# Performance work log

Hardware: AMD Instinct MI355X
Metric: run time of the kernel (lower is better)

## Reference

```python
import jax, jax.numpy as jnp
import numpy as np

N = 50000
E = 800000
DESC = 256
IN_CH = DESC + 64  # 320
HEADS = 4
HC = 64  # hidden_channels // heads
HID = HEADS * HC  # 256


def _lin(k, fan_in, fan_out):
    kw, kb = jax.random.split(k)
    s = 1.0 / np.sqrt(fan_in)
    W = jax.random.uniform(kw, (fan_in, fan_out), minval=-s, maxval=s, dtype=jnp.float32)
    b = jax.random.uniform(kb, (fan_out,), minval=-s, maxval=s, dtype=jnp.float32)
    return W, b


def setup_inputs() -> dict:
    key = jax.random.key(0)
    ks = jax.random.split(key, 16)
    x = jax.random.normal(ks[0], (N, DESC), dtype=jnp.float32)
    kpts = jax.random.uniform(ks[1], (N, 2), dtype=jnp.float32) * jnp.array([1216.0, 352.0])
    pts_3d = jax.random.uniform(ks[2], (N, 3), dtype=jnp.float32) * 10.0
    edge_index = jax.random.randint(ks[3], (2, E), 0, N, dtype=jnp.int64)

    W1, b1 = _lin(ks[4], 3, 32)
    W2, b2 = _lin(ks[5], 32, 64)
    Wres, bres = _lin(ks[6], IN_CH, HID)
    Wl, bl = _lin(ks[7], IN_CH, HID)
    Wr, br = _lin(ks[8], IN_CH, HID)
    We, _ = _lin(ks[9], 3, HID)
    att = jax.random.normal(ks[10], (HEADS, HC), dtype=jnp.float32) * 0.1
    conv_bias = jnp.zeros((HID,), dtype=jnp.float32)
    gamma = jnp.ones((HID,), dtype=jnp.float32)
    beta = jnp.zeros((HID,), dtype=jnp.float32)
    Wp, bp = _lin(ks[11], HID, 256)
    return dict(x=x, kpts=kpts, pts_3d=pts_3d, edge_index=edge_index,
                W1=W1, b1=b1, W2=W2, b2=b2, Wres=Wres, bres=bres,
                Wl=Wl, bl=bl, Wr=Wr, br=br, We=We, att=att, conv_bias=conv_bias,
                gamma=gamma, beta=beta, Wp=Wp, bp=bp)


def reference(x, kpts, pts_3d, edge_index, W1, b1, W2, b2, Wres, bres,
              Wl, bl, Wr, br, We, att, conv_bias, gamma, beta, Wp, bp):
    n = x.shape[0]
    norm_uv = kpts / jnp.array([1216.0, 352.0], dtype=kpts.dtype)
    depth = pts_3d[:, 2:3]
    pos_input = jnp.concatenate([norm_uv, depth], axis=-1)  # [N,3]
    pos_feat = jax.nn.silu(pos_input @ W1 + b1) @ W2 + b2   # [N,64]
    node_x = jnp.concatenate([x, pos_feat], axis=-1)        # [N,320]

    src, dst = edge_index[0], edge_index[1]
    rel_uv = norm_uv[dst] - norm_uv[src]                    # [E,2]
    dist = jnp.linalg.norm(rel_uv, axis=-1, keepdims=True)  # [E,1]
    edge_attr = jnp.concatenate([rel_uv, dist], axis=-1)    # [E,3]

    identity = node_x @ Wres + bres                         # [N,256]

    # GATv2Conv (share_weights=False, concat=True, neg_slope=0.2, no self-loops)
    x_l = (node_x @ Wl + bl).reshape(n, HEADS, HC)
    x_r = (node_x @ Wr + br).reshape(n, HEADS, HC)
    e_feat = (edge_attr @ We).reshape(-1, HEADS, HC)        # [E,H,C]

    m = x_l[src] + x_r[dst] + e_feat                        # [E,H,C]
    m = jnp.where(m >= 0, m, 0.2 * m)                       # LeakyReLU(0.2)
    logits = jnp.einsum('ehc,hc->eh', m, att)               # [E,H]

    # segment softmax over incoming edges of each dst node
    lmax = jax.ops.segment_max(logits, dst, num_segments=n)  # [N,H]
    ex = jnp.exp(logits - lmax[dst])
    denom = jax.ops.segment_sum(ex, dst, num_segments=n)     # [N,H]
    alpha = ex / (denom[dst] + 1e-16)                        # [E,H]

    msg = x_l[src] * alpha[:, :, None]                       # [E,H,C]
    out = jax.ops.segment_sum(msg, dst, num_segments=n).reshape(n, HID) + conv_bias

    # LayerNorm
    mu = out.mean(-1, keepdims=True)
    var = out.var(-1, keepdims=True)
    out = (out - mu) / jnp.sqrt(var + 1e-5) * gamma + beta

    out = jax.nn.silu(out)
    out = out + identity
    out = out @ Wp + bp
    return out, alpha
```

## Files before the change

kernel.cpp:

```cpp
#include <hip/hip_runtime.h>
#include <math.h>

#define NN 50000
#define NPAD 50048
#define EE 800000
#define HIDC 256
#define INCH 320

typedef __attribute__((ext_vector_type(8))) short bf16x8;
typedef __attribute__((ext_vector_type(4))) float f32x4;
typedef __attribute__((ext_vector_type(2))) float f32x2;

static __device__ __forceinline__ float4 ld4(const float* p){ return *(const float4*)p; }

static __device__ __forceinline__ unsigned short f2b(float f){
  union { float f; unsigned u; } v; v.f = f;
  unsigned r = v.u + 0x7fffu + ((v.u >> 16) & 1u);
  return (unsigned short)(r >> 16);
}
static __device__ __forceinline__ float b2f(unsigned short u){
  union { unsigned u; float f; } v; v.u = ((unsigned)u) << 16; return v.f;
}
static __device__ __forceinline__ f32x2 unpk(unsigned u){
  f32x2 r;
  r.x = __uint_as_float(u << 16);
  r.y = __uint_as_float(u & 0xffff0000u);
  return r;
}
static __device__ __forceinline__ f32x2 fma2(f32x2 a, f32x2 b, f32x2 c){
  return __builtin_elementwise_fma(a, b, c);
}
static __device__ __forceinline__ f32x2 max2(f32x2 a, f32x2 b){
  return __builtin_elementwise_max(a, b);
}
static __device__ __forceinline__ f32x2 set2(float v){ f32x2 r; r.x = v; r.y = v; return r; }

typedef const __attribute__((address_space(1))) unsigned int* gas_u32;
typedef __attribute__((address_space(3))) unsigned int* las_u32;
static __device__ __forceinline__ void gload_lds16(const void* g, void* l){
  __builtin_amdgcn_global_load_lds((gas_u32)g, (las_u32)l, 16, 0, 0);
}

__global__ void cvt_x_kernel(const float* __restrict__ x, unsigned short* __restrict__ nodex)
{
  int t = blockIdx.x*blockDim.x + threadIdx.x;
  int row = t >> 6;
  if (row >= NN) return;
  int c4 = (t & 63) * 4;
  float4 v = ld4(x + (size_t)row*256 + c4);
  ushort4 o;
  o.x = f2b(v.x); o.y = f2b(v.y); o.z = f2b(v.z); o.w = f2b(v.w);
  *(ushort4*)(nodex + (size_t)row*320 + c4) = o;
}

__global__ void node_mlp_kernel(const float* __restrict__ kpts,
                                const float* __restrict__ pts3d,
                                const float* __restrict__ W1, const float* __restrict__ b1,
                                const float* __restrict__ W2, const float* __restrict__ b2,
                                unsigned short* __restrict__ nodex)
{
  int i = blockIdx.x*blockDim.x + threadIdx.x;
  if (i >= NN) return;
  float u = kpts[2*i]   * (1.0f/1216.0f);
  float v = kpts[2*i+1] * (1.0f/352.0f);
  float d = pts3d[3*i+2];
  float h[32];
#pragma unroll
  for (int j=0;j<32;++j){
    float t = u*W1[j] + v*W1[32+j] + d*W1[64+j] + b1[j];
    h[j] = t / (1.0f + __expf(-t));
  }
  for (int o=0;o<64;o+=4){
    float s0=b2[o], s1=b2[o+1], s2=b2[o+2], s3=b2[o+3];
#pragma unroll
    for (int j=0;j<32;++j){
      float hj = h[j];
      const float* w = W2 + j*64 + o;
      s0 += hj*w[0]; s1 += hj*w[1]; s2 += hj*w[2]; s3 += hj*w[3];
    }
    ushort4 r; r.x=f2b(s0); r.y=f2b(s1); r.z=f2b(s2); r.w=f2b(s3);
    *(ushort4*)(nodex + (size_t)i*320 + 256 + o) = r;
  }
}

__global__ void cvt_w_kernel(const float* __restrict__ Wres, const float* __restrict__ Wl,
                             const float* __restrict__ Wr,   const float* __restrict__ Wp,
                             const float* __restrict__ bres, const float* __restrict__ bl,
                             const float* __restrict__ br,
                             unsigned short* __restrict__ wt, float* __restrict__ biascat)
{
  int t = blockIdx.x*blockDim.x + threadIdx.x;
  if (t < 245760) {
    int which = t / 81920;
    int rem = t % 81920;
    int n = rem / 320, k = rem % 320;
    const float* W = (which == 0) ? Wres : (which == 1) ? Wl : Wr;
    wt[(size_t)which*81920 + rem] = f2b(W[(size_t)k*256 + n]);
  } else if (t < 311296) {
    int r = t - 245760;
    int n = r / 256, k = r % 256;
    wt[245760 + r] = f2b(Wp[(size_t)k*256 + n]);
  } else {
    int r = t - 311296;
    const float* src = (r < 256) ? bres : (r < 512) ? bl : br;
    biascat[r] = src[r & 255];
  }
}

#define GK 32
__global__ __launch_bounds__(256) void mfma_gemm_kernel(
    const unsigned short* __restrict__ A,
    const unsigned short* __restrict__ BT,
    const float* __restrict__ bias,
    float* __restrict__ Cf,
    unsigned short* __restrict__ Cx1,
    unsigned short* __restrict__ Cx2,
    int M, int K)
{
  __shared__ unsigned short Als[128*GK];
  __shared__ unsigned short Bls[128*GK];
  int tid = threadIdx.x;
  int lane = tid & 63, wave = tid >> 6;
  int wm = (wave >> 1) * 64, wn = (wave & 1) * 64;
  int row0 = blockIdx.x * 128, col0 = blockIdx.y * 128;

  f32x4 acc[4][4];
#pragma unroll
  for (int i=0;i<4;++i)
#pragma unroll
    for (int j=0;j<4;++j){ acc[i][j].x=0.f; acc[i][j].y=0.f; acc[i][j].z=0.f; acc[i][j].w=0.f; }

  int fm = lane & 15;
  int fk = (lane >> 4) * 8;

  for (int k0 = 0; k0 < K; k0 += GK) {
#pragma unroll
    for (int it = 0; it < 2; ++it) {
      int seg = it*256 + tid;
      int r = seg >> 2, kb = (seg & 3) * 8;
      gload_lds16(A  + (size_t)(row0 + r)*K + k0 + kb, Als + (it*256 + wave*64)*8);
      gload_lds16(BT + (size_t)(col0 + r)*K + k0 + kb, Bls + (it*256 + wave*64)*8);
    }
    __syncthreads();

    bf16x8 af[4], bfr[4];
#pragma unroll
    for (int mi=0; mi<4; ++mi)
      af[mi] = *(const bf16x8*)&Als[(wm + mi*16 + fm)*GK + fk];
#pragma unroll
    for (int ni=0; ni<4; ++ni)
      bfr[ni] = *(const bf16x8*)&Bls[(wn + ni*16 + fm)*GK + fk];
#pragma unroll
    for (int mi=0; mi<4; ++mi)
#pragma unroll
      for (int ni=0; ni<4; ++ni)
        acc[mi][ni] = __builtin_amdgcn_mfma_f32_16x16x32_bf16(af[mi], bfr[ni], acc[mi][ni], 0, 0, 0);
    __syncthreads();
  }

  int seg = col0 >> 8;
  int colbase = col0 - seg*256;
  int cn = lane & 15, cr = (lane >> 4) * 4;
#pragma unroll
  for (int ni=0; ni<4; ++ni){
    int gcol = col0 + wn + ni*16 + cn;
    int col  = colbase + wn + ni*16 + cn;
    float bb = bias[gcol];
#pragma unroll
    for (int mi=0; mi<4; ++mi){
#pragma unroll
      for (int r=0; r<4; ++r){
        int row = row0 + wm + mi*16 + cr + r;
        if (row < M){
          float v = acc[mi][ni][r] + bb;
          if (seg == 0)      Cf [(size_t)row*256 + col] = v;
          else if (seg == 1) Cx1[(size_t)row*256 + col] = f2b(v);
          else               Cx2[(size_t)row*256 + col] = f2b(v);
        }
      }
    }
  }
}

__global__ void hist_kernel(const int* __restrict__ ei, int* __restrict__ deg){
  int e = blockIdx.x*blockDim.x + threadIdx.x;
  if (e < EE) atomicAdd(&deg[ei[EE + e]], 1);
}

__global__ __launch_bounds__(1024) void scan1_kernel(const int* __restrict__ deg,
                                                     int* __restrict__ incl, int* __restrict__ bsum){
  __shared__ int wsums[16];
  int t = threadIdx.x, lane = t & 63, w = t >> 6;
  int i = blockIdx.x*1024 + t;
  int v = (i < NN) ? deg[i] : 0;
  int sc = v;
#pragma unroll
  for (int off = 1; off < 64; off <<= 1) {
    int o = __shfl_up(sc, off, 64);
    if (lane >= off) sc += o;
  }
  if (lane == 63) wsums[w] = sc;
  __syncthreads();
  if (w == 0) {
    int ws = (lane < 16) ? wsums[lane] : 0;
#pragma unroll
    for (int off = 1; off < 16; off <<= 1) {
      int o = __shfl_up(ws, off, 64);
      if (lane >= off) ws += o;
    }
    if (lane < 16) wsums[lane] = ws;
  }
  __syncthreads();
  int woff = (w > 0) ? wsums[w-1] : 0;
  if (i < NN) incl[i] = sc + woff;
  if (t == 1023) bsum[blockIdx.x] = woff + sc;
}

__global__ void scan2_kernel(int* __restrict__ bsum, int nblk){
  int lane = threadIdx.x;
  int v = (lane < nblk) ? bsum[lane] : 0;
#pragma unroll
  for (int off = 1; off < 64; off <<= 1) {
    int o = __shfl_up(v, off, 64);
    if (lane >= off) v += o;
  }
  if (lane < nblk) bsum[lane] = v;
}

__global__ __launch_bounds__(1024) void scan3_kernel(const int* __restrict__ incl,
                                                     const int* __restrict__ deg,
                                                     const int* __restrict__ bsum,
                                                     int* __restrict__ rowptr, int* __restrict__ cursor,
                                                     int nblk){
  int i = blockIdx.x*1024 + threadIdx.x;
  if (i < NN) {
    int b = blockIdx.x;
    int prev = (b > 0) ? bsum[b-1] : 0;
    int ex = prev + incl[i] - deg[i];
    rowptr[i] = ex;
    cursor[i] = ex;
  }
  if (i == 0) rowptr[NN] = bsum[nblk-1];
}

__global__ void scatter_kernel(const int* __restrict__ ei, const float* __restrict__ kpts,
                               int* __restrict__ cursor,
                               float4* __restrict__ edata, int* __restrict__ eord){
  int e = blockIdx.x*blockDim.x + threadIdx.x;
  if (e >= EE) return;
  int s = ei[e];
  int d = ei[EE + e];
  int pos = atomicAdd(&cursor[d], 1);
  float su = kpts[2*s]   * (1.0f/1216.0f);
  float sv = kpts[2*s+1] * (1.0f/352.0f);
  float du = kpts[2*d]   * (1.0f/1216.0f);
  float dv = kpts[2*d+1] * (1.0f/352.0f);
  float ru = du - su, rv = dv - sv;
  float dist = sqrtf(ru*ru + rv*rv);
  float4 ed; ed.x = ru; ed.y = rv; ed.z = dist; ed.w = __int_as_float(s);
  edata[pos] = ed;
  eord[pos] = e;
}


#define LOAD_ED(P, ED, EV)                                           \
  {                                                                  \
    int j_ = 2*(P) + half;                                           \
    int idx_ = rs + ((j_ < deg) ? j_ : 0);                           \
    ED = edata[idx_];                                                \
    EV = eord[idx_];                                                 \
  }

#define LOAD_Q(ED, Q)                                                \
  {                                                                  \
    int s_ = __float_as_int((ED).w);                                 \
    Q = *(const uint4*)(xlp + ((size_t)s_ << 8));                    \
  }

#define PROC_E(P, ED, EV, Q)                                         \
  {                                                                  \
    bool act = (2*(P) + half) < deg;                                 \
    f32x2 x0 = unpk((Q).x), x1 = unpk((Q).y);                        \
    f32x2 x2 = unpk((Q).z), x3 = unpk((Q).w);                        \
    f32x2 ru = set2((ED).x), rv = set2((ED).y), dd = set2((ED).z);   \
    f32x2 t0 = fma2(ru, w0[0], xr4[0]);                              \
    f32x2 t1 = fma2(ru, w0[1], xr4[1]);                              \
    f32x2 t2 = fma2(ru, w0[2], xr4[2]);                              \
    f32x2 t3 = fma2(ru, w0[3], xr4[3]);                              \
    t0 = fma2(rv, w1[0], t0); t1 = fma2(rv, w1[1], t1);              \
    t2 = fma2(rv, w1[2], t2); t3 = fma2(rv, w1[3], t3);              \
    t0 = fma2(dd, w2[0], t0); t1 = fma2(dd, w2[1], t1);              \
    t2 = fma2(dd, w2[2], t2); t3 = fma2(dd, w2[3], t3);              \
    t0 = t0 + x0; t1 = t1 + x1; t2 = t2 + x2; t3 = t3 + x3;          \
    t0 = max2(t0, t0*0.2f); t1 = max2(t1, t1*0.2f);                  \
    t2 = max2(t2, t2*0.2f); t3 = max2(t3, t3*0.2f);                  \
    f32x2 pd = t0*at4[0];                                            \
    pd = fma2(t1, at4[1], pd);                                       \
    pd = fma2(t2, at4[2], pd);                                       \
    pd = fma2(t3, at4[3], pd);                                       \
    float p = pd.x + pd.y;                                           \
    p += __shfl_xor(p, 1, 64);                                       \
    p += __shfl_xor(p, 2, 64);                                       \
    p += __shfl_xor(p, 4, 64);                                       \
    float exv = act ? __expf(p) : 0.0f;                              \
    denom += exv;                                                    \
    if (act && (li & 7) == 0)                                        \
      alpha_out[(size_t)(EV)*4 + head] = exv;                        \
    f32x2 ex2 = set2(exv);                                           \
    agg[0] = fma2(ex2, x0, agg[0]); agg[1] = fma2(ex2, x1, agg[1]);  \
    agg[2] = fma2(ex2, x2, agg[2]); agg[3] = fma2(ex2, x3, agg[3]);  \
  }

__global__ __launch_bounds__(256) void node_attn_kernel(
    const float4* __restrict__ edata, const int* __restrict__ eord,
    const unsigned short* __restrict__ xl, const unsigned short* __restrict__ xr,
    const float* __restrict__ We, const float* __restrict__ att,
    const float* __restrict__ cbias, const float* __restrict__ gamma,
    const float* __restrict__ beta,
    const int* __restrict__ rowptr,
    const float* __restrict__ identity,
    float* __restrict__ alpha_out, float* __restrict__ denom_buf,
    unsigned short* __restrict__ hbuf)
{
  int wid  = threadIdx.x >> 6;
  int lane = threadIdx.x & 63;
  int v = blockIdx.x*4 + wid;
  if (v >= NN) return;
  int li   = lane & 31;
  int half = lane >> 5;
  int c0   = li * 8;
  int head = li >> 3;

  f32x2 w0[4], w1[4], w2[4], at4[4], xr4[4];
  {
    float4 a = ld4(We + c0),        b = ld4(We + c0 + 4);
    w0[0].x=a.x; w0[0].y=a.y; w0[1].x=a.z; w0[1].y=a.w;
    w0[2].x=b.x; w0[2].y=b.y; w0[3].x=b.z; w0[3].y=b.w;
    a = ld4(We + 256 + c0); b = ld4(We + 256 + c0 + 4);
    w1[0].x=a.x; w1[0].y=a.y; w1[1].x=a.z; w1[1].y=a.w;
    w1[2].x=b.x; w1[2].y=b.y; w1[3].x=b.z; w1[3].y=b.w;
    a = ld4(We + 512 + c0); b = ld4(We + 512 + c0 + 4);
    w2[0].x=a.x; w2[0].y=a.y; w2[1].x=a.z; w2[1].y=a.w;
    w2[2].x=b.x; w2[2].y=b.y; w2[3].x=b.z; w2[3].y=b.w;
    a = ld4(att + c0);      b = ld4(att + c0 + 4);
    at4[0].x=a.x; at4[0].y=a.y; at4[1].x=a.z; at4[1].y=a.w;
    at4[2].x=b.x; at4[2].y=b.y; at4[3].x=b.z; at4[3].y=b.w;
  }
  {
    uint4 xrq = *(const uint4*)(xr + (size_t)v*256 + c0);
    xr4[0] = unpk(xrq.x); xr4[1] = unpk(xrq.y);
    xr4[2] = unpk(xrq.z); xr4[3] = unpk(xrq.w);
  }
  const unsigned short* xlp = xl + c0;

  int rs = rowptr[v], re = rowptr[v+1];
  int deg = re - rs;
  int npairs = (deg + 1) >> 1;

  float denom = 0.f;
  f32x2 agg[4];
  agg[0]=set2(0.f); agg[1]=set2(0.f); agg[2]=set2(0.f); agg[3]=set2(0.f);

  if (npairs > 0) {
    float4 ed0, ed1, ed2;
    int e0 = 0, e1 = 0, e2 = 0;
    uint4 q0, q1;
    ed1.x=0.f; ed1.y=0.f; ed1.z=0.f; ed1.w=0.f; ed2 = ed1;
    q1.x=0u; q1.y=0u; q1.z=0u; q1.w=0u;

    LOAD_ED(0, ed0, e0);
    LOAD_Q(ed0, q0);
    if (npairs > 1) { LOAD_ED(1, ed1, e1); }

    for (int p = 0; p < npairs; ++p) {
      if (p + 2 < npairs) { LOAD_ED(p+2, ed2, e2); }
      if (p + 1 < npairs) { LOAD_Q(ed1, q1); }
      PROC_E(p, ed0, e0, q0);
      ed0 = ed1; e0 = e1; q0 = q1;
      ed1 = ed2; e1 = e2;
    }
  }

#pragma unroll
  for (int k = 0; k < 4; ++k) {
    agg[k].x += __shfl_xor(agg[k].x, 32, 64);
    agg[k].y += __shfl_xor(agg[k].y, 32, 64);
  }
  denom += __shfl_xor(denom, 32, 64);
  if (half == 0 && (li & 7) == 0) denom_buf[(size_t)v*4 + head] = denom;
  float rdenom = 1.0f / (denom + 1e-16f);

  float4 cb0 = ld4(cbias + c0), cb1 = ld4(cbias + c0 + 4);
  float a0 = agg[0].x*rdenom + cb0.x;
  float a1 = agg[0].y*rdenom + cb0.y;
  float a2 = agg[1].x*rdenom + cb0.z;
  float a3 = agg[1].y*rdenom + cb0.w;
  float a4 = agg[2].x*rdenom + cb1.x;
  float a5 = agg[2].y*rdenom + cb1.y;
  float a6 = agg[3].x*rdenom + cb1.z;
  float a7 = agg[3].y*rdenom + cb1.w;

  float ps  = ((a0+a1)+(a2+a3)) + ((a4+a5)+(a6+a7));
  float ps2 = ((a0*a0+a1*a1)+(a2*a2+a3*a3)) + ((a4*a4+a5*a5)+(a6*a6+a7*a7));
#pragma unroll
  for (int off = 1; off < 32; off <<= 1) {
    ps  += __shfl_xor(ps,  off, 64);
    ps2 += __shfl_xor(ps2, off, 64);
  }
  float mu  = ps  * (1.0f/256.0f);
  float var = ps2 * (1.0f/256.0f) - mu*mu;
  float rstd = rsqrtf(var + 1e-5f);
  float4 g0  = ld4(gamma + c0), g1 = ld4(gamma + c0 + 4);
  float4 bb0 = ld4(beta  + c0), bb1 = ld4(beta  + c0 + 4);
  float4 id0 = ld4(identity + (size_t)v*256 + c0);
  float4 id1 = ld4(identity + (size_t)v*256 + c0 + 4);

  float y0 = (a0 - mu)*rstd*g0.x + bb0.x;
  float y1 = (a1 - mu)*rstd*g0.y + bb0.y;
  float y2 = (a2 - mu)*rstd*g0.z + bb0.z;
  float y3 = (a3 - mu)*rstd*g0.w + bb0.w;
  float y4 = (a4 - mu)*rstd*g1.x + bb1.x;
  float y5 = (a5 - mu)*rstd*g1.y + bb1.y;
  float y6 = (a6 - mu)*rstd*g1.z + bb1.z;
  float y7 = (a7 - mu)*rstd*g1.w + bb1.w;
  y0 = y0 / (1.0f + __expf(-y0)) + id0.x;
  y1 = y1 / (1.0f + __expf(-y1)) + id0.y;
  y2 = y2 / (1.0f + __expf(-y2)) + id0.z;
  y3 = y3 / (1.0f + __expf(-y3)) + id0.w;
  y4 = y4 / (1.0f + __expf(-y4)) + id1.x;
  y5 = y5 / (1.0f + __expf(-y5)) + id1.y;
  y6 = y6 / (1.0f + __expf(-y6)) + id1.z;
  y7 = y7 / (1.0f + __expf(-y7)) + id1.w;

  if (half == 0) {
    uint4 hq;
    hq.x = (unsigned)f2b(y0) | ((unsigned)f2b(y1) << 16);
    hq.y = (unsigned)f2b(y2) | ((unsigned)f2b(y3) << 16);
    hq.z = (unsigned)f2b(y4) | ((unsigned)f2b(y5) << 16);
    hq.w = (unsigned)f2b(y6) | ((unsigned)f2b(y7) << 16);
    *(uint4*)(hbuf + (size_t)v*256 + c0) = hq;
  }
}

__global__ void alpha_fin_kernel(const int* __restrict__ ei, const float* __restrict__ denom_buf,
                                 float* __restrict__ alpha)
{
  int e = blockIdx.x*blockDim.x + threadIdx.x;
  if (e >= EE) return;
  int d = ei[EE + e];
  float4 dn = ld4(denom_buf + (size_t)d*4);
  float4 a = ld4(alpha + (size_t)e*4);
  a.x /= (dn.x + 1e-16f);
  a.y /= (dn.y + 1e-16f);
  a.z /= (dn.z + 1e-16f);
  a.w /= (dn.w + 1e-16f);
  *(float4*)(alpha + (size_t)e*4) = a;
}

extern "C" void kernel_launch(void* const* d_in, const int* in_sizes, int n_in,
                              void* d_out, int out_size, void* d_ws, size_t ws_size,
                              hipStream_t stream)
{
  const float* x      = (const float*)d_in[0];
  const float* kpts   = (const float*)d_in[1];
  const float* pts3d  = (const float*)d_in[2];
  const int*   ei     = (const int*)d_in[3];
  const float* W1     = (const float*)d_in[4];
  const float* b1     = (const float*)d_in[5];
  const float* W2     = (const float*)d_in[6];
  const float* b2     = (const float*)d_in[7];
  const float* Wres   = (const float*)d_in[8];
  const float* bres   = (const float*)d_in[9];
  const float* Wl     = (const float*)d_in[10];
  const float* bl     = (const float*)d_in[11];
  const float* Wr     = (const float*)d_in[12];
  const float* br     = (const float*)d_in[13];
  const float* We     = (const float*)d_in[14];
  const float* att    = (const float*)d_in[15];
  const float* cbias  = (const float*)d_in[16];
  const float* gamma  = (const float*)d_in[17];
  const float* beta   = (const float*)d_in[18];
  const float* Wp     = (const float*)d_in[19];
  const float* bp     = (const float*)d_in[20];

  float* out       = (float*)d_out;
  float* alpha_out = out + (size_t)NN*HIDC;

  float* wsf = (float*)d_ws;
  float*          identity = wsf;
  unsigned short* xl       = (unsigned short*)(wsf + 12800000);
  unsigned short* xr       = (unsigned short*)(wsf + 19206144);
  unsigned short* nodex    = (unsigned short*)(wsf + 25612288);
  unsigned short* hbuf     = (unsigned short*)(wsf + 25612288);
  unsigned short* wt       = (unsigned short*)(wsf + 33619968);
  float*          biascat  = wsf + 33775616;
  float*          denomb   = wsf + 33776384;
  float4*         edata    = (float4*)(wsf + 33976384);
  int*            eord     = (int*)(wsf + 37176384);
  int*            incl     = (int*)(wsf + 37176384);
  int*            deg      = (int*)(wsf + 37976384);
  int*            rowptr   = (int*)(wsf + 38026384);
  int*            cursor   = (int*)(wsf + 38076385);
  int*            bsum     = (int*)(wsf + 38126385);

  unsigned short* wtcat = wt;
  unsigned short* wtp   = wt + 245760;

  cvt_x_kernel<<<12500, 256, 0, stream>>>(x, nodex);
  node_mlp_kernel<<<(NN+255)/256, 256, 0, stream>>>(kpts, pts3d, W1, b1, W2, b2, nodex);
  cvt_w_kernel<<<1219, 256, 0, stream>>>(Wres, Wl, Wr, Wp, bres, bl, br, wt, biascat);

  dim3 g3(NPAD/128, 6);
  mfma_gemm_kernel<<<g3, 256, 0, stream>>>(nodex, wtcat, biascat, identity, xl, xr, NN, INCH);

  hipMemsetAsync(deg, 0, NN*sizeof(int), stream);
  hist_kernel<<<(EE+255)/256, 256, 0, stream>>>(ei, deg);
  int nblk = (NN + 1023) / 1024;
  scan1_kernel<<<nblk, 1024, 0, stream>>>(deg, incl, bsum);
  scan2_kernel<<<1, 64, 0, stream>>>(bsum, nblk);
  scan3_kernel<<<nblk, 1024, 0, stream>>>(incl, deg, bsum, rowptr, cursor, nblk);
  scatter_kernel<<<(EE+255)/256, 256, 0, stream>>>(ei, kpts, cursor, edata, eord);

  node_attn_kernel<<<(NN+3)/4, 256, 0, stream>>>(edata, eord, xl, xr, We, att,
                                                 cbias, gamma, beta,
                                                 rowptr, identity,
                                                 alpha_out, denomb, hbuf);
  alpha_fin_kernel<<<(EE+255)/256, 256, 0, stream>>>(ei, denomb, alpha_out);

  dim3 g1(NPAD/128, 2);
  mfma_gemm_kernel<<<g1, 256, 0, stream>>>(hbuf, wtp, bp, out, nullptr, nullptr, NN, HIDC);
}
```

Measured before the change: 564.3 us.

## Deepen gather prefetch to four-pair double-buffered batches in node attention loop

Replaces the one-pair-ahead software pipeline in the per-node attention loop with two register banks of four edge pairs each. The next batch of edge data and source-row gathers is issued before the current batch is processed, so more memory loads are in flight per wave. The edge-order index is no longer carried in registers and is read directly when the alpha value is stored. This raises register pressure, which may cut occupancy, and does redundant clamped loads for low-degree nodes (average degree is 16).

```diff
diff --git a/kernel.cpp b/kernel.cpp
--- a/kernel.cpp
+++ b/kernel.cpp
@@ -263,12 +263,11 @@
 }
 
 
-#define LOAD_ED(P, ED, EV)                                           \
+#define LOAD_ED(P, ED)                                               \
   {                                                                  \
     int j_ = 2*(P) + half;                                           \
     int idx_ = rs + ((j_ < deg) ? j_ : 0);                           \
     ED = edata[idx_];                                                \
-    EV = eord[idx_];                                                 \
   }
 
 #define LOAD_Q(ED, Q)                                                \
@@ -277,9 +276,10 @@
     Q = *(const uint4*)(xlp + ((size_t)s_ << 8));                    \
   }
 
-#define PROC_E(P, ED, EV, Q)                                         \
+#define PROC_E(P, ED, Q)                                             \
   {                                                                  \
-    bool act = (2*(P) + half) < deg;                                 \
+    int jj_ = 2*(P) + half;                                          \
+    bool act = jj_ < deg;                                            \
     f32x2 x0 = unpk((Q).x), x1 = unpk((Q).y);                        \
     f32x2 x2 = unpk((Q).z), x3 = unpk((Q).w);                        \
     f32x2 ru = set2((ED).x), rv = set2((ED).y), dd = set2((ED).z);   \
@@ -305,7 +305,7 @@
     float exv = act ? __expf(p) : 0.0f;                              \
     denom += exv;                                                    \
     if (act && (li & 7) == 0)                                        \
-      alpha_out[(size_t)(EV)*4 + head] = exv;                        \
+      alpha_out[(size_t)eop[jj_]*4 + head] = exv;                    \
     f32x2 ex2 = set2(exv);                                           \
     agg[0] = fma2(ex2, x0, agg[0]); agg[1] = fma2(ex2, x1, agg[1]);  \
     agg[2] = fma2(ex2, x2, agg[2]); agg[3] = fma2(ex2, x3, agg[3]);  \
@@ -356,28 +356,44 @@
   int rs = rowptr[v], re = rowptr[v+1];
   int deg = re - rs;
   int npairs = (deg + 1) >> 1;
+  const int* eop = eord + rs;
 
   float denom = 0.f;
   f32x2 agg[4];
   agg[0]=set2(0.f); agg[1]=set2(0.f); agg[2]=set2(0.f); agg[3]=set2(0.f);
 
   if (npairs > 0) {
-    float4 ed0, ed1, ed2;
-    int e0 = 0, e1 = 0, e2 = 0;
-    uint4 q0, q1;
-    ed1.x=0.f; ed1.y=0.f; ed1.z=0.f; ed1.w=0.f; ed2 = ed1;
-    q1.x=0u; q1.y=0u; q1.z=0u; q1.w=0u;
-
-    LOAD_ED(0, ed0, e0);
-    LOAD_Q(ed0, q0);
-    if (npairs > 1) { LOAD_ED(1, ed1, e1); }
-
-    for (int p = 0; p < npairs; ++p) {
-      if (p + 2 < npairs) { LOAD_ED(p+2, ed2, e2); }
-      if (p + 1 < npairs) { LOAD_Q(ed1, q1); }
-      PROC_E(p, ed0, e0, q0);
-      ed0 = ed1; e0 = e1; q0 = q1;
-      ed1 = ed2; e1 = e2;
+    float4 edA0, edA1, edA2, edA3;
+    float4 edB0, edB1, edB2, edB3;
+    uint4 qA0, qA1, qA2, qA3;
+    uint4 qB0, qB1, qB2, qB3;
+
+    LOAD_ED(0, edA0); LOAD_ED(1, edA1); LOAD_ED(2, edA2); LOAD_ED(3, edA3);
+    LOAD_Q(edA0, qA0); LOAD_Q(edA1, qA1); LOAD_Q(edA2, qA2); LOAD_Q(edA3, qA3);
+
+    int p = 0;
+    while (true) {
+      if (p + 4 < npairs) {
+        LOAD_ED(p+4, edB0); LOAD_ED(p+5, edB1);
+        LOAD_ED(p+6, edB2); LOAD_ED(p+7, edB3);
+        LOAD_Q(edB0, qB0); LOAD_Q(edB1, qB1);
+        LOAD_Q(edB2, qB2); LOAD_Q(edB3, qB3);
+      }
+      PROC_E(p+0, edA0, qA0); PROC_E(p+1, edA1, qA1);
+      PROC_E(p+2, edA2, qA2); PROC_E(p+3, edA3, qA3);
+      p += 4;
+      if (p >= npairs) break;
+
+      if (p + 4 < npairs) {
+        LOAD_ED(p+4, edA0); LOAD_ED(p+5, edA1);
+        LOAD_ED(p+6, edA2); LOAD_ED(p+7, edA3);
+        LOAD_Q(edA0, qA0); LOAD_Q(edA1, qA1);
+        LOAD_Q(edA2, qA2); LOAD_Q(edA3, qA3);
+      }
+      PROC_E(p+0, edB0, qB0); PROC_E(p+1, edB1, qB1);
+      PROC_E(p+2, edB2, qB2); PROC_E(p+3, edB3, qB3);
+      p += 4;
+      if (p >= npairs) break;
     }
   }
 
```

Result: slower. 644.9 us (+14.3%).
